# Performance work log

Hardware: AMD Instinct MI355X
Metric: run time of the kernel (lower is better)

## Reference

```python
import jax, jax.numpy as jnp
import numpy as np
from jax import lax

N_SAMPLES = 2 ** 15      # 32768
D_SIZE = 256             # number of dictionary atoms
KERNEL = 256             # atom length
N_STEPS = 16             # sparse_coding_iterations
CHANNELS = 128


def setup_inputs() -> dict:
    key = jax.random.key(0)
    ks = jax.random.split(key, 9)
    B = 8
    x = jax.random.normal(ks[0], (B, N_SAMPLES), dtype=jnp.float32)
    # dictionary, initialized uniform(-1, 1) as in nn.Parameter(...).uniform_(-1, 1)
    d = jax.random.uniform(ks[1], (D_SIZE, KERNEL), dtype=jnp.float32, minval=-1.0, maxval=1.0)
    # 1x1 Conv1d weights stored as (out, in); biases (out,)
    w_pos_amp = jax.random.normal(ks[2], (CHANNELS, 2), dtype=jnp.float32) * 0.1
    b_pos_amp = jnp.zeros((CHANNELS,), dtype=jnp.float32)
    w_atoms = jax.random.normal(ks[3], (CHANNELS, D_SIZE), dtype=jnp.float32) * 0.05
    b_atoms = jnp.zeros((CHANNELS,), dtype=jnp.float32)
    w_reduce = jax.random.normal(ks[4], (CHANNELS, 2 * CHANNELS), dtype=jnp.float32) * 0.05
    b_reduce = jnp.zeros((CHANNELS,), dtype=jnp.float32)
    return {
        'x': x, 'd': d,
        'w_pos_amp': w_pos_amp, 'b_pos_amp': b_pos_amp,
        'w_atoms': w_atoms, 'b_atoms': b_atoms,
        'w_reduce': w_reduce, 'b_reduce': b_reduce,
    }


def _correlate(residual, d):
    # residual: (B, 1, N), d: (D, K) -> feature map (B, D, N-K+1) (valid cross-correlation,
    # identical to torch F.conv1d with no padding)
    return lax.conv_general_dilated(
        residual, d[:, None, :], window_strides=(1,), padding='VALID',
        dimension_numbers=('NCH', 'OIH', 'NCH'))


def _matching_pursuit(x3, d):
    """16-step greedy matching pursuit. Returns key points (B, 2+D, N_STEPS) and residual."""
    B = x3.shape[0]
    T = N_SAMPLES - KERNEL + 1  # valid correlation length

    def step(residual, _):
        fm = _correlate(residual, d)                       # (B, D, T)
        flat = fm.reshape(B, -1)
        idx = jnp.argmax(jnp.abs(flat), axis=1)            # best (atom, pos) per example
        amp = jnp.take_along_axis(flat, idx[:, None], axis=1)[:, 0]
        atom_idx = idx // T
        pos = idx % T

        def subtract(r, p, ai, a):
            seg = lax.dynamic_slice(r, (p,), (KERNEL,))
            return lax.dynamic_update_slice(r, seg - a * d[ai], (p,))

        new_res = jax.vmap(subtract)(residual[:, 0, :], pos, atom_idx, amp)[:, None, :]
        enc = jnp.concatenate([
            (pos.astype(jnp.float32) / T)[:, None],        # normalized position
            amp[:, None],                                  # amplitude
            jax.nn.one_hot(atom_idx, D_SIZE, dtype=jnp.float32),  # atom one-hot
        ], axis=1)                                         # (B, 2+D)
        return new_res, enc

    residual, encs = lax.scan(step, x3, None, length=N_STEPS)  # encs: (S, B, 2+D)
    kp = jnp.transpose(encs, (1, 2, 0))                        # (B, 2+D, S)
    return kp, residual


def _conv1x1(w, b, x):
    # w: (O, C), x: (B, C, T) -> (B, O, T)
    return jnp.einsum('oc,bct->bot', w, x) + b[None, :, None]


def reference(x, d, w_pos_amp, b_pos_amp, w_atoms, b_atoms, w_reduce, b_reduce):
    B = x.shape[0]
    x3 = x.reshape(B, 1, N_SAMPLES)
    kp, _ = _matching_pursuit(x3, d)          # (B, 258, 16)
    pos_amp = kp[:, :2, :]
    atoms = kp[:, 2:, :]
    pa = _conv1x1(w_pos_amp, b_pos_amp, pos_amp)
    at = _conv1x1(w_atoms, b_atoms, atoms)
    h = jnp.concatenate([pa, at], axis=1)     # (B, 2*channels, 16)
    return _conv1x1(w_reduce, b_reduce, h)    # (B, channels, 16)
```

## Files before the change

### kernel.cpp

```cpp
#include <hip/hip_runtime.h>
#include <hip/hip_bf16.h>
#include <float.h>

#define NS 32768
#define KER 256
#define TOUT 32513
#define NATOM 256
#define NSTEP 16
#define BATCH 8
#define NBLK 255
#define XSTR 33024
#define SW4(i) ((i) + (((i) >> 5) << 2))

typedef __attribute__((ext_vector_type(8))) _Float16 half8;
typedef __attribute__((ext_vector_type(4))) float f32x4;
typedef __attribute__((ext_vector_type(4))) unsigned int uint4v;

__device__ __forceinline__ void cmax(float& ba, float& bs, float& bi,
                                     float oa, float os, float oi) {
    if (oa > ba || (oa == ba && oi < bi)) { ba = oa; bs = os; bi = oi; }
}

__device__ __forceinline__ void fma8(float acc[8], float4 dA, float4 dB,
                                     float4 w0, float4 w1, float4 w2, float4 w3) {
    float w[16] = {w0.x,w0.y,w0.z,w0.w, w1.x,w1.y,w1.z,w1.w,
                   w2.x,w2.y,w2.z,w2.w, w3.x,w3.y,w3.z,w3.w};
    float dv[8] = {dA.x,dA.y,dA.z,dA.w, dB.x,dB.y,dB.z,dB.w};
#pragma unroll
    for (int i = 0; i < 8; ++i)
#pragma unroll
        for (int j = 0; j < 8; ++j)
            acc[j] = fmaf(dv[i], w[i + j], acc[j]);
}

__global__ __launch_bounds__(256) void k_prep(const float* __restrict__ x,
                                              const float* __restrict__ d,
                                              unsigned int* __restrict__ xp,
                                              unsigned short* __restrict__ dh,
                                              unsigned short* __restrict__ dl) {
    const int gid = blockIdx.x * 256 + threadIdx.x;
    const int NX = BATCH * XSTR;
    if (gid < NX) {
        const int b = gid / XSTR, i = gid - b * XSTR;
        const float v = (i < NS) ? x[b * NS + i] : 0.f;
        const _Float16 h = (_Float16)v;
        const _Float16 lo = (_Float16)(v - (float)h);
        xp[gid] = ((unsigned int)__builtin_bit_cast(unsigned short, lo) << 16)
                | (unsigned int)__builtin_bit_cast(unsigned short, h);
    } else {
        const int j = gid - NX;
        if (j < NATOM * KER) {
            const float v = d[j];
            const _Float16 h = (_Float16)v;
            const _Float16 lo = (_Float16)(v - (float)h);
            dh[j] = __builtin_bit_cast(unsigned short, h);
            dl[j] = __builtin_bit_cast(unsigned short, lo);
        }
    }
}

__global__ __launch_bounds__(256) void k_init(const unsigned int* __restrict__ xp,
                                              const unsigned short* __restrict__ dh,
                                              const unsigned short* __restrict__ dl,
                                              float4* __restrict__ bm) {
    const int c = blockIdx.x, mg = blockIdx.y, b = blockIdx.z;
    const int tid = threadIdx.x;
    const int w = tid >> 6, l = tid & 63;
    const int l15 = l & 15, g = l >> 4;
    __shared__ unsigned int xw[512];
    __shared__ float4 wmax[4][16];
    const int t0 = c << 8;
    xw[tid] = xp[b * XSTR + t0 + tid];
    xw[tid + 256] = xp[b * XSTR + t0 + 256 + tid];
    __syncthreads();

    f32x4 acc0 = {0.f,0.f,0.f,0.f}, acc1 = {0.f,0.f,0.f,0.f};
    f32x4 acc2 = {0.f,0.f,0.f,0.f}, acc3 = {0.f,0.f,0.f,0.f};
    const int arow = (mg << 4) + l15;
    const unsigned short* dhp = dh + arow * 256 + (g << 3);
    const unsigned short* dlp = dl + arow * 256 + (g << 3);

#pragma unroll 2
    for (int kk = 0; kk < 8; ++kk) {
        const half8 ah = *(const half8*)(dhp + (kk << 5));
        const half8 al = *(const half8*)(dlp + (kk << 5));
        const int sbase = (w << 6) + (kk << 5) + l15 + (g << 3);
#pragma unroll
        for (int nt = 0; nt < 4; ++nt) {
            const int s = sbase + (nt << 4);
            const unsigned int w0 = xw[s],     w1 = xw[s + 1];
            const unsigned int w2 = xw[s + 2], w3 = xw[s + 3];
            const unsigned int w4 = xw[s + 4], w5 = xw[s + 5];
            const unsigned int w6 = xw[s + 6], w7 = xw[s + 7];
            uint4v hv = { (w0 & 0xffffu) | (w1 << 16),
                          (w2 & 0xffffu) | (w3 << 16),
                          (w4 & 0xffffu) | (w5 << 16),
                          (w6 & 0xffffu) | (w7 << 16) };
            uint4v lv = { (w0 >> 16) | (w1 & 0xffff0000u),
                          (w2 >> 16) | (w3 & 0xffff0000u),
                          (w4 >> 16) | (w5 & 0xffff0000u),
                          (w6 >> 16) | (w7 & 0xffff0000u) };
            const half8 bh = __builtin_bit_cast(half8, hv);
            const half8 bl = __builtin_bit_cast(half8, lv);
            f32x4 a = (nt == 0) ? acc0 : (nt == 1) ? acc1 : (nt == 2) ? acc2 : acc3;
            a = __builtin_amdgcn_mfma_f32_16x16x32_f16(ah, bl, a, 0, 0, 0);
            a = __builtin_amdgcn_mfma_f32_16x16x32_f16(al, bh, a, 0, 0, 0);
            a = __builtin_amdgcn_mfma_f32_16x16x32_f16(ah, bh, a, 0, 0, 0);
            if (nt == 0) acc0 = a; else if (nt == 1) acc1 = a;
            else if (nt == 2) acc2 = a; else acc3 = a;
        }
    }

#pragma unroll
    for (int r = 0; r < 4; ++r) {
        float ba = -1.f, bsg = 0.f, bi = 3.0e7f;
        const int atomg = (mg << 4) + (g << 2) + r;
#pragma unroll
        for (int nt = 0; nt < 4; ++nt) {
            const int t = t0 + (w << 6) + (nt << 4) + l15;
            const float v = (nt == 0) ? acc0[r] : (nt == 1) ? acc1[r]
                          : (nt == 2) ? acc2[r] : acc3[r];
            const float av = fabsf(v);
            if (t < TOUT && av > ba) { ba = av; bsg = v; bi = (float)(atomg * TOUT + t); }
        }
#pragma unroll
        for (int m = 1; m <= 8; m <<= 1) {
            float oa = __shfl_xor(ba, m, 16);
            float os = __shfl_xor(bsg, m, 16);
            float oi = __shfl_xor(bi, m, 16);
            cmax(ba, bsg, bi, oa, os, oi);
        }
        if (l15 == 0) wmax[w][(g << 2) + r] = make_float4(ba, bsg, bi, 0.f);
    }
    __syncthreads();
    if (tid < 32) {
        const int a = tid & 15, p = tid >> 4;
        float4 e1 = wmax[2 * p][a];
        const float4 e2 = wmax[2 * p + 1][a];
        float ba = e1.x, bsg = e1.y, bi = e1.z;
        cmax(ba, bsg, bi, e2.x, e2.y, e2.z);
        const int blk = (c << 1) + p;
        if (blk < NBLK)
            bm[(size_t)((b << 8) + (mg << 4) + a) * NBLK + blk] =
                make_float4(ba, bsg, bi, 0.f);
    }
}

__global__ __launch_bounds__(256) void k_lvl2(const float4* __restrict__ bm,
                                              float4* __restrict__ l2) {
    const int b = blockIdx.y;
    const int oglob = blockIdx.x * 8 + (threadIdx.x >> 5);
    const int lane = threadIdx.x & 31;
    const float4* row = bm + (size_t)(b * NATOM + oglob) * NBLK;
    float ba = -1.f, bsg = 0.f, bi = 3.0e7f;
    for (int i = lane; i < NBLK; i += 32) {
        float4 e = row[i];
        cmax(ba, bsg, bi, e.x, e.y, e.z);
    }
#pragma unroll
    for (int m = 16; m >= 1; m >>= 1) {
        float oa = __shfl_xor(ba, m, 32);
        float os = __shfl_xor(bsg, m, 32);
        float oi = __shfl_xor(bi, m, 32);
        cmax(ba, bsg, bi, oa, os, oi);
    }
    if (lane == 0) l2[(b << 8) + oglob] = make_float4(ba, bsg, bi, 0.f);
}

__global__ __launch_bounds__(512) void k_step(const float* __restrict__ x,
                                              const float* __restrict__ d,
                                              float4* __restrict__ bm,
                                              float4* __restrict__ l2,
                                              int* __restrict__ pos_a,
                                              int* __restrict__ atom_a,
                                              float* __restrict__ amp_a,
                                              int step) {
    const int og = blockIdx.x, b = blockIdx.y;
    const int tid = threadIdx.x;
    const int wave = tid >> 6, lane = tid & 63;
    __shared__ float dt[2048];
    __shared__ float rsu[1024];
    __shared__ float4 sred[8];
    __shared__ float4 upd[8][5];
    __shared__ int s_pos[NSTEP], s_atom[NSTEP];
    __shared__ float s_amp[NSTEP];

    ((float4*)dt)[tid] = ((const float4*)(d + og * 2048))[tid];
    if (tid < step) {
        s_pos[tid]  = pos_a[tid * BATCH + b];
        s_atom[tid] = atom_a[tid * BATCH + b];
        s_amp[tid]  = amp_a[tid * BATCH + b];
    }
    const float4* l2r = l2 + (step & 1) * (BATCH * NATOM);
    float4*       l2w = l2 + ((step + 1) & 1) * (BATCH * NATOM);

    {
        float ba = -1.f, bsg = 0.f, bi = 3.0e7f;
        if (tid < 256) {
            float4 e = l2r[(b << 8) + tid];
            ba = e.x; bsg = e.y; bi = e.z;
        }
#pragma unroll
        for (int m = 32; m >= 1; m >>= 1) {
            float oa = __shfl_xor(ba, m);
            float os = __shfl_xor(bsg, m);
            float oi = __shfl_xor(bi, m);
            cmax(ba, bsg, bi, oa, os, oi);
        }
        if (lane == 0) sred[wave] = make_float4(ba, bsg, bi, 0.f);
    }
    __syncthreads();
    if (tid == 0) {
        float4 r = sred[0];
#pragma unroll
        for (int i = 1; i < 8; ++i) {
            float4 q = sred[i];
            if (q.x > r.x || (q.x == r.x && q.z < r.z)) r = q;
        }
        const int idx = (int)r.z;
        const int atom = idx / TOUT;
        const int pos = idx - atom * TOUT;
        s_pos[step] = pos; s_atom[step] = atom; s_amp[step] = r.y;
        if (og == 0) {
            pos_a[step * BATCH + b] = pos;
            atom_a[step * BATCH + b] = atom;
            amp_a[step * BATCH + b] = r.y;
        }
    }
    __syncthreads();

    const int p = s_pos[step];
    int tlo = p - 255; if (tlo < 0) tlo = 0;
    int thi = p + 255; if (thi > TOUT - 1) thi = TOUT - 1;
    const int bs0 = tlo >> 7, be0 = thi >> 7;
    const int rbase = bs0 << 7;
    const int nblks = be0 - bs0 + 1;
    const int rlen = (nblks << 7) + 255;
    for (int i = tid; i < rlen; i += 512) {
        const int g = rbase + i;
        float v = (g < NS) ? x[(size_t)b * NS + g] : 0.f;
        for (int s2 = 0; s2 <= step; ++s2) {
            const int off = g - s_pos[s2];
            if (off >= 0 && off < KER)
                v = __fsub_rn(v, __fmul_rn(s_amp[s2], d[s_atom[s2] * KER + off]));
        }
        rsu[SW4(i)] = v;
    }
    __syncthreads();

    const int lg = lane >> 4, l16 = lane & 15;
    const float* dp = dt + (wave << 8) + (lg << 6);
    const int atomg = (og << 3) + wave;
    for (int bb = 0; bb < nblks; ++bb) {
        const int blk = bs0 + bb;
        const int t0r = (bb << 7) + (l16 << 3) + (lg << 6);
        float acc[8];
#pragma unroll
        for (int j = 0; j < 8; ++j) acc[j] = 0.f;
        float4 A0 = *(const float4*)(rsu + SW4(t0r));
        float4 A1 = *(const float4*)(rsu + SW4(t0r + 4));
        float4 B0 = *(const float4*)(rsu + SW4(t0r + 8));
        float4 B1 = *(const float4*)(rsu + SW4(t0r + 12));
#pragma unroll
        for (int kk = 0; kk < 64; kk += 16) {
            float4 d0 = *(const float4*)(dp + kk);
            float4 d1 = *(const float4*)(dp + kk + 4);
            float4 N0 = *(const float4*)(rsu + SW4(t0r + kk + 16));
            float4 N1 = *(const float4*)(rsu + SW4(t0r + kk + 20));
            fma8(acc, d0, d1, A0, A1, B0, B1);
            float4 d2 = *(const float4*)(dp + kk + 8);
            float4 d3 = *(const float4*)(dp + kk + 12);
            float4 M0 = *(const float4*)(rsu + SW4(t0r + kk + 24));
            float4 M1 = *(const float4*)(rsu + SW4(t0r + kk + 28));
            fma8(acc, d2, d3, B0, B1, N0, N1);
            A0 = N0; A1 = N1; B0 = M0; B1 = M1;
        }
#pragma unroll
        for (int j = 0; j < 8; ++j) {
            acc[j] += __shfl_xor(acc[j], 16);
            acc[j] += __shfl_xor(acc[j], 32);
        }
        float ba = -1.f, bsg = 0.f, bi = 3.0e7f;
        const int tb = rbase + (bb << 7) + (l16 << 3);
#pragma unroll
        for (int j = 0; j < 8; ++j) {
            const int t = tb + j;
            const float av = fabsf(acc[j]);
            if (t < TOUT && av > ba) { ba = av; bsg = acc[j]; bi = (float)(atomg * TOUT + t); }
        }
#pragma unroll
        for (int m = 32; m >= 1; m >>= 1) {
            float oa = __shfl_xor(ba, m);
            float os = __shfl_xor(bsg, m);
            float oi = __shfl_xor(bi, m);
            cmax(ba, bsg, bi, oa, os, oi);
        }
        if (lane == 0) {
            float4 e4 = make_float4(ba, bsg, bi, 0.f);
            bm[(size_t)(b * NATOM + atomg) * NBLK + blk] = e4;
            upd[wave][bb] = e4;
        }
    }
    __syncthreads();

    {
        float ba = -1.f, bsg = 0.f, bi = 3.0e7f;
        const float4* row = bm + (size_t)(b * NATOM + atomg) * NBLK;
        for (int i = lane; i < NBLK; i += 64) {
            float4 e2 = (i >= bs0 && i <= be0) ? upd[wave][i - bs0] : row[i];
            cmax(ba, bsg, bi, e2.x, e2.y, e2.z);
        }
#pragma unroll
        for (int m = 32; m >= 1; m >>= 1) {
            float oa = __shfl_xor(ba, m);
            float os = __shfl_xor(bsg, m);
            float oi = __shfl_xor(bi, m);
            cmax(ba, bsg, bi, oa, os, oi);
        }
        if (lane == 0) l2w[(b << 8) + atomg] = make_float4(ba, bsg, bi, 0.f);
    }
}

__global__ __launch_bounds__(128) void k_head(const int* __restrict__ pos_a,
                                              const int* __restrict__ atom_a,
                                              const float* __restrict__ amp_a,
                                              const float4* __restrict__ l2,
                                              const float* __restrict__ wpa,
                                              const float* __restrict__ bpa,
                                              const float* __restrict__ wat,
                                              const float* __restrict__ bat,
                                              const float* __restrict__ wr,
                                              const float* __restrict__ br,
                                              float* __restrict__ out) {
    const int s = blockIdx.x, b = blockIdx.y;
    const int o = threadIdx.x;
    __shared__ float4 hred[2];
    __shared__ int sh_pos, sh_atom;
    __shared__ float sh_amp;
    int pos, atom; float amp;
    if (s == NSTEP - 1) {
        const float4* l2r = l2 + ((NSTEP - 1) & 1) * (BATCH * NATOM);
        float ba = -1.f, bsg = 0.f, bi = 3.0e7f;
        float4 e0 = l2r[(b << 8) + o];
        float4 e1 = l2r[(b << 8) + 128 + o];
        cmax(ba, bsg, bi, e0.x, e0.y, e0.z);
        cmax(ba, bsg, bi, e1.x, e1.y, e1.z);
#pragma unroll
        for (int m = 32; m >= 1; m >>= 1) {
            float oa = __shfl_xor(ba, m);
            float os = __shfl_xor(bsg, m);
            float oi = __shfl_xor(bi, m);
            cmax(ba, bsg, bi, oa, os, oi);
        }
        if ((o & 63) == 0) hred[o >> 6] = make_float4(ba, bsg, bi, 0.f);
        __syncthreads();
        if (o == 0) {
            float4 r = hred[0], q = hred[1];
            if (q.x > r.x || (q.x == r.x && q.z < r.z)) r = q;
            const int idx = (int)r.z;
            sh_atom = idx / TOUT;
            sh_pos = idx - sh_atom * TOUT;
            sh_amp = r.y;
        }
        __syncthreads();
        pos = sh_pos; atom = sh_atom; amp = sh_amp;
    } else {
        pos  = pos_a[s * BATCH + b];
        atom = atom_a[s * BATCH + b];
        amp  = amp_a[s * BATCH + b];
    }
    const float posn = (float)pos / 32513.0f;
    float sum = br[o];
    for (int c = 0; c < 128; ++c) {
        float pa = wpa[c * 2] * posn + wpa[c * 2 + 1] * amp + bpa[c];
        float at = wat[c * 256 + atom] + bat[c];
        sum += wr[o * 256 + c] * pa + wr[o * 256 + 128 + c] * at;
    }
    out[(b * 128 + o) * NSTEP + s] = sum;
}

extern "C" void kernel_launch(void* const* d_in, const int* in_sizes, int n_in,
                              void* d_out, int out_size, void* d_ws, size_t ws_size,
                              hipStream_t stream) {
    const float* x   = (const float*)d_in[0];
    const float* d   = (const float*)d_in[1];
    const float* wpa = (const float*)d_in[2];
    const float* bpa = (const float*)d_in[3];
    const float* wat = (const float*)d_in[4];
    const float* bat = (const float*)d_in[5];
    const float* wr  = (const float*)d_in[6];
    const float* br  = (const float*)d_in[7];
    float* out = (float*)d_out;

    char* ws = (char*)d_ws;
    float4* bm = (float4*)ws;
    float4* l2 = (float4*)(ws + 8355840);
    int*   pos_a  = (int*)(ws + 8355840 + 65536);
    int*   atom_a = pos_a + NSTEP * BATCH;
    float* amp_a  = (float*)(atom_a + NSTEP * BATCH);
    unsigned int*   xp = (unsigned int*)(ws + 8355840 + 65536 + 512);
    unsigned short* dh = (unsigned short*)(ws + 8355840 + 65536 + 512 + 1056768);
    unsigned short* dl = dh + NATOM * KER;

    const int prep_n = BATCH * XSTR + NATOM * KER;
    k_prep<<<(prep_n + 255) / 256, 256, 0, stream>>>(x, d, xp, dh, dl);
    k_init<<<dim3(128, 16, 8), 256, 0, stream>>>(xp, dh, dl, bm);
    k_lvl2<<<dim3(32, 8), 256, 0, stream>>>(bm, l2);
    for (int st = 0; st < NSTEP - 1; ++st)
        k_step<<<dim3(32, 8), 512, 0, stream>>>(x, d, bm, l2, pos_a, atom_a, amp_a, st);
    k_head<<<dim3(16, 8), 128, 0, stream>>>(pos_a, atom_a, amp_a, l2,
                                            wpa, bpa, wat, bat, wr, br, out);
}
```

Baseline: 433.6 us.

## Use 32x32 MFMA in init, shrink block-max records, ping-pong materialized residual

The initial correlation kernel now uses 32x32x16 fp16 MFMAs over 32-atom groups, reading x from split hi/lo uint2 planes and d from a pre-swizzled layout. Per-block max records shrink from float4 to float2, with the absolute value recomputed on read, which halves bm traffic. The step kernel no longer replays every prior subtraction from x. It keeps a materialized residual in two ping-pong buffers, and each launch copies and updates it with only the current atom. This adds a full residual copy per step and a device-to-device memcpy at the start, in exchange for removing the O(step) replay loop.

```diff
diff --git a/kernel.cpp b/kernel.cpp
--- a/kernel.cpp
+++ b/kernel.cpp
@@ -13,7 +13,7 @@
 #define SW4(i) ((i) + (((i) >> 5) << 2))
 
 typedef __attribute__((ext_vector_type(8))) _Float16 half8;
-typedef __attribute__((ext_vector_type(4))) float f32x4;
+typedef __attribute__((ext_vector_type(16))) float f32x16;
 typedef __attribute__((ext_vector_type(4))) unsigned int uint4v;
 
 __device__ __forceinline__ void cmax(float& ba, float& bs, float& bi,
@@ -33,143 +33,166 @@
             acc[j] = fmaf(dv[i], w[i + j], acc[j]);
 }
 
+__device__ __forceinline__ unsigned short f16hi(float v) {
+    return __builtin_bit_cast(unsigned short, (_Float16)v);
+}
+__device__ __forceinline__ unsigned short f16lo(float v) {
+    const _Float16 h = (_Float16)v;
+    return __builtin_bit_cast(unsigned short, (_Float16)(v - (float)h));
+}
+
 __global__ __launch_bounds__(256) void k_prep(const float* __restrict__ x,
                                               const float* __restrict__ d,
-                                              unsigned int* __restrict__ xp,
-                                              unsigned short* __restrict__ dh,
-                                              unsigned short* __restrict__ dl) {
+                                              uint2* __restrict__ xh4,
+                                              uint2* __restrict__ xl4,
+                                              uint4* __restrict__ dhF,
+                                              uint4* __restrict__ dlF) {
     const int gid = blockIdx.x * 256 + threadIdx.x;
-    const int NX = BATCH * XSTR;
-    if (gid < NX) {
+    const int NXE = BATCH * XSTR;
+    if (gid < NXE) {
         const int b = gid / XSTR, i = gid - b * XSTR;
-        const float v = (i < NS) ? x[b * NS + i] : 0.f;
-        const _Float16 h = (_Float16)v;
-        const _Float16 lo = (_Float16)(v - (float)h);
-        xp[gid] = ((unsigned int)__builtin_bit_cast(unsigned short, lo) << 16)
-                | (unsigned int)__builtin_bit_cast(unsigned short, h);
+        float v[4];
+#pragma unroll
+        for (int u = 0; u < 4; ++u)
+            v[u] = (i + u < NS) ? x[b * NS + i + u] : 0.f;
+        uint2 hw, lw;
+        hw.x = (unsigned int)f16hi(v[0]) | ((unsigned int)f16hi(v[1]) << 16);
+        hw.y = (unsigned int)f16hi(v[2]) | ((unsigned int)f16hi(v[3]) << 16);
+        lw.x = (unsigned int)f16lo(v[0]) | ((unsigned int)f16lo(v[1]) << 16);
+        lw.y = (unsigned int)f16lo(v[2]) | ((unsigned int)f16lo(v[3]) << 16);
+        xh4[gid] = hw; xl4[gid] = lw;
     } else {
-        const int j = gid - NX;
-        if (j < NATOM * KER) {
-            const float v = d[j];
-            const _Float16 h = (_Float16)v;
-            const _Float16 lo = (_Float16)(v - (float)h);
-            dh[j] = __builtin_bit_cast(unsigned short, h);
-            dl[j] = __builtin_bit_cast(unsigned short, lo);
-        }
-    }
-}
-
-__global__ __launch_bounds__(256) void k_init(const unsigned int* __restrict__ xp,
-                                              const unsigned short* __restrict__ dh,
-                                              const unsigned short* __restrict__ dl,
-                                              float4* __restrict__ bm) {
+        const int j = gid - NXE;
+        if (j < NATOM * 32) {
+            const int kg = j >> 8, atom = j & 255;
+            const float* dp = d + atom * 256 + (kg << 3);
+            uint4 hw, lw;
+            hw.x = (unsigned int)f16hi(dp[0]) | ((unsigned int)f16hi(dp[1]) << 16);
+            hw.y = (unsigned int)f16hi(dp[2]) | ((unsigned int)f16hi(dp[3]) << 16);
+            hw.z = (unsigned int)f16hi(dp[4]) | ((unsigned int)f16hi(dp[5]) << 16);
+            hw.w = (unsigned int)f16hi(dp[6]) | ((unsigned int)f16hi(dp[7]) << 16);
+            lw.x = (unsigned int)f16lo(dp[0]) | ((unsigned int)f16lo(dp[1]) << 16);
+            lw.y = (unsigned int)f16lo(dp[2]) | ((unsigned int)f16lo(dp[3]) << 16);
+            lw.z = (unsigned int)f16lo(dp[4]) | ((unsigned int)f16lo(dp[5]) << 16);
+            lw.w = (unsigned int)f16lo(dp[6]) | ((unsigned int)f16lo(dp[7]) << 16);
+            dhF[(kg << 8) + atom] = hw;
+            dlF[(kg << 8) + atom] = lw;
+        }
+    }
+}
+
+__global__ __launch_bounds__(256) void k_init(const uint2* __restrict__ xh4,
+                                              const uint2* __restrict__ xl4,
+                                              const uint4* __restrict__ dhF,
+                                              const uint4* __restrict__ dlF,
+                                              float2* __restrict__ bm) {
     const int c = blockIdx.x, mg = blockIdx.y, b = blockIdx.z;
     const int tid = threadIdx.x;
     const int w = tid >> 6, l = tid & 63;
-    const int l15 = l & 15, g = l >> 4;
-    __shared__ unsigned int xw[512];
-    __shared__ float4 wmax[4][16];
+    const int n = l & 31, h = l >> 5;
+    __shared__ uint2 xh[512], xl[512];
+    __shared__ float4 wmax[4][32];
     const int t0 = c << 8;
-    xw[tid] = xp[b * XSTR + t0 + tid];
-    xw[tid + 256] = xp[b * XSTR + t0 + 256 + tid];
-    __syncthreads();
-
-    f32x4 acc0 = {0.f,0.f,0.f,0.f}, acc1 = {0.f,0.f,0.f,0.f};
-    f32x4 acc2 = {0.f,0.f,0.f,0.f}, acc3 = {0.f,0.f,0.f,0.f};
-    const int arow = (mg << 4) + l15;
-    const unsigned short* dhp = dh + arow * 256 + (g << 3);
-    const unsigned short* dlp = dl + arow * 256 + (g << 3);
-
+    for (int i = tid; i < 512; i += 256) {
+        xh[i] = xh4[b * XSTR + t0 + i];
+        xl[i] = xl4[b * XSTR + t0 + i];
+    }
+    __syncthreads();
+
+    const int arow = (mg << 5) + n;
+    f32x16 acc0 = {0.f}, acc1 = {0.f};
+#pragma unroll
+    for (int j = 0; j < 16; ++j) { acc0[j] = 0.f; acc1[j] = 0.f; }
+    const int sb = (w << 6) + n + (h << 3);
 #pragma unroll 2
-    for (int kk = 0; kk < 8; ++kk) {
-        const half8 ah = *(const half8*)(dhp + (kk << 5));
-        const half8 al = *(const half8*)(dlp + (kk << 5));
-        const int sbase = (w << 6) + (kk << 5) + l15 + (g << 3);
-#pragma unroll
-        for (int nt = 0; nt < 4; ++nt) {
-            const int s = sbase + (nt << 4);
-            const unsigned int w0 = xw[s],     w1 = xw[s + 1];
-            const unsigned int w2 = xw[s + 2], w3 = xw[s + 3];
-            const unsigned int w4 = xw[s + 4], w5 = xw[s + 5];
-            const unsigned int w6 = xw[s + 6], w7 = xw[s + 7];
-            uint4v hv = { (w0 & 0xffffu) | (w1 << 16),
-                          (w2 & 0xffffu) | (w3 << 16),
-                          (w4 & 0xffffu) | (w5 << 16),
-                          (w6 & 0xffffu) | (w7 << 16) };
-            uint4v lv = { (w0 >> 16) | (w1 & 0xffff0000u),
-                          (w2 >> 16) | (w3 & 0xffff0000u),
-                          (w4 >> 16) | (w5 & 0xffff0000u),
-                          (w6 >> 16) | (w7 & 0xffff0000u) };
+    for (int kk = 0; kk < 16; ++kk) {
+        const int kg = (kk << 1) + h;
+        const half8 ah = __builtin_bit_cast(half8, dhF[(kg << 8) + arow]);
+        const half8 al = __builtin_bit_cast(half8, dlF[(kg << 8) + arow]);
+        const int s0 = sb + (kk << 4);
+        {
+            const uint2 h0 = xh[s0], h1 = xh[s0 + 4];
+            const uint2 l0 = xl[s0], l1 = xl[s0 + 4];
+            const uint4v hv = {h0.x, h0.y, h1.x, h1.y};
+            const uint4v lv = {l0.x, l0.y, l1.x, l1.y};
             const half8 bh = __builtin_bit_cast(half8, hv);
             const half8 bl = __builtin_bit_cast(half8, lv);
-            f32x4 a = (nt == 0) ? acc0 : (nt == 1) ? acc1 : (nt == 2) ? acc2 : acc3;
-            a = __builtin_amdgcn_mfma_f32_16x16x32_f16(ah, bl, a, 0, 0, 0);
-            a = __builtin_amdgcn_mfma_f32_16x16x32_f16(al, bh, a, 0, 0, 0);
-            a = __builtin_amdgcn_mfma_f32_16x16x32_f16(ah, bh, a, 0, 0, 0);
-            if (nt == 0) acc0 = a; else if (nt == 1) acc1 = a;
-            else if (nt == 2) acc2 = a; else acc3 = a;
-        }
-    }
-
-#pragma unroll
-    for (int r = 0; r < 4; ++r) {
+            acc0 = __builtin_amdgcn_mfma_f32_32x32x16_f16(ah, bl, acc0, 0, 0, 0);
+            acc0 = __builtin_amdgcn_mfma_f32_32x32x16_f16(al, bh, acc0, 0, 0, 0);
+            acc0 = __builtin_amdgcn_mfma_f32_32x32x16_f16(ah, bh, acc0, 0, 0, 0);
+        }
+        {
+            const uint2 h0 = xh[s0 + 32], h1 = xh[s0 + 36];
+            const uint2 l0 = xl[s0 + 32], l1 = xl[s0 + 36];
+            const uint4v hv = {h0.x, h0.y, h1.x, h1.y};
+            const uint4v lv = {l0.x, l0.y, l1.x, l1.y};
+            const half8 bh = __builtin_bit_cast(half8, hv);
+            const half8 bl = __builtin_bit_cast(half8, lv);
+            acc1 = __builtin_amdgcn_mfma_f32_32x32x16_f16(ah, bl, acc1, 0, 0, 0);
+            acc1 = __builtin_amdgcn_mfma_f32_32x32x16_f16(al, bh, acc1, 0, 0, 0);
+            acc1 = __builtin_amdgcn_mfma_f32_32x32x16_f16(ah, bh, acc1, 0, 0, 0);
+        }
+    }
+
+    const int tb0 = t0 + (w << 6) + n;
+#pragma unroll
+    for (int r = 0; r < 16; ++r) {
+        const int atom_l = (r & 3) + ((r >> 2) << 3) + (h << 2);
+        const float fa = (float)(((mg << 5) + atom_l) * TOUT);
         float ba = -1.f, bsg = 0.f, bi = 3.0e7f;
-        const int atomg = (mg << 4) + (g << 2) + r;
-#pragma unroll
-        for (int nt = 0; nt < 4; ++nt) {
-            const int t = t0 + (w << 6) + (nt << 4) + l15;
-            const float v = (nt == 0) ? acc0[r] : (nt == 1) ? acc1[r]
-                          : (nt == 2) ? acc2[r] : acc3[r];
-            const float av = fabsf(v);
-            if (t < TOUT && av > ba) { ba = av; bsg = v; bi = (float)(atomg * TOUT + t); }
-        }
-#pragma unroll
-        for (int m = 1; m <= 8; m <<= 1) {
-            float oa = __shfl_xor(ba, m, 16);
-            float os = __shfl_xor(bsg, m, 16);
-            float oi = __shfl_xor(bi, m, 16);
+        const float v0 = acc0[r], v1 = acc1[r];
+        if (tb0 < TOUT) { ba = fabsf(v0); bsg = v0; bi = fa + (float)tb0; }
+        if (tb0 + 32 < TOUT) {
+            const float a1 = fabsf(v1);
+            if (a1 > ba) { ba = a1; bsg = v1; bi = fa + (float)(tb0 + 32); }
+        }
+#pragma unroll
+        for (int m = 1; m <= 16; m <<= 1) {
+            const float oa = __shfl_xor(ba, m, 32);
+            const float os = __shfl_xor(bsg, m, 32);
+            const float oi = __shfl_xor(bi, m, 32);
             cmax(ba, bsg, bi, oa, os, oi);
         }
-        if (l15 == 0) wmax[w][(g << 2) + r] = make_float4(ba, bsg, bi, 0.f);
-    }
-    __syncthreads();
-    if (tid < 32) {
-        const int a = tid & 15, p = tid >> 4;
-        float4 e1 = wmax[2 * p][a];
-        const float4 e2 = wmax[2 * p + 1][a];
+        if (n == 0) wmax[w][atom_l] = make_float4(ba, bsg, bi, 0.f);
+    }
+    __syncthreads();
+    if (tid < 64) {
+        const int a = tid & 31, p = tid >> 5;
+        const float4 e1 = wmax[(p << 1)][a];
+        const float4 e2 = wmax[(p << 1) + 1][a];
         float ba = e1.x, bsg = e1.y, bi = e1.z;
         cmax(ba, bsg, bi, e2.x, e2.y, e2.z);
         const int blk = (c << 1) + p;
         if (blk < NBLK)
-            bm[(size_t)((b << 8) + (mg << 4) + a) * NBLK + blk] =
-                make_float4(ba, bsg, bi, 0.f);
-    }
-}
-
-__global__ __launch_bounds__(256) void k_lvl2(const float4* __restrict__ bm,
+            bm[(size_t)((b << 8) + (mg << 5) + a) * NBLK + blk] = make_float2(bsg, bi);
+    }
+}
+
+__global__ __launch_bounds__(256) void k_lvl2(const float2* __restrict__ bm,
                                               float4* __restrict__ l2) {
     const int b = blockIdx.y;
     const int oglob = blockIdx.x * 8 + (threadIdx.x >> 5);
     const int lane = threadIdx.x & 31;
-    const float4* row = bm + (size_t)(b * NATOM + oglob) * NBLK;
+    const float2* row = bm + (size_t)(b * NATOM + oglob) * NBLK;
     float ba = -1.f, bsg = 0.f, bi = 3.0e7f;
     for (int i = lane; i < NBLK; i += 32) {
-        float4 e = row[i];
-        cmax(ba, bsg, bi, e.x, e.y, e.z);
+        const float2 e = row[i];
+        cmax(ba, bsg, bi, fabsf(e.x), e.x, e.y);
     }
 #pragma unroll
     for (int m = 16; m >= 1; m >>= 1) {
-        float oa = __shfl_xor(ba, m, 32);
-        float os = __shfl_xor(bsg, m, 32);
-        float oi = __shfl_xor(bi, m, 32);
+        const float oa = __shfl_xor(ba, m, 32);
+        const float os = __shfl_xor(bsg, m, 32);
+        const float oi = __shfl_xor(bi, m, 32);
         cmax(ba, bsg, bi, oa, os, oi);
     }
     if (lane == 0) l2[(b << 8) + oglob] = make_float4(ba, bsg, bi, 0.f);
 }
 
-__global__ __launch_bounds__(512) void k_step(const float* __restrict__ x,
-                                              const float* __restrict__ d,
-                                              float4* __restrict__ bm,
+__global__ __launch_bounds__(512) void k_step(const float* __restrict__ d,
+                                              const float* __restrict__ resid_src,
+                                              float* __restrict__ resid_dst,
+                                              float2* __restrict__ bm,
                                               float4* __restrict__ l2,
                                               int* __restrict__ pos_a,
                                               int* __restrict__ atom_a,
@@ -182,29 +205,24 @@
     __shared__ float rsu[1024];
     __shared__ float4 sred[8];
     __shared__ float4 upd[8][5];
-    __shared__ int s_pos[NSTEP], s_atom[NSTEP];
-    __shared__ float s_amp[NSTEP];
+    __shared__ int sh_pos, sh_atom;
+    __shared__ float sh_amp;
 
     ((float4*)dt)[tid] = ((const float4*)(d + og * 2048))[tid];
-    if (tid < step) {
-        s_pos[tid]  = pos_a[tid * BATCH + b];
-        s_atom[tid] = atom_a[tid * BATCH + b];
-        s_amp[tid]  = amp_a[tid * BATCH + b];
-    }
     const float4* l2r = l2 + (step & 1) * (BATCH * NATOM);
     float4*       l2w = l2 + ((step + 1) & 1) * (BATCH * NATOM);
 
     {
         float ba = -1.f, bsg = 0.f, bi = 3.0e7f;
         if (tid < 256) {
-            float4 e = l2r[(b << 8) + tid];
+            const float4 e = l2r[(b << 8) + tid];
             ba = e.x; bsg = e.y; bi = e.z;
         }
 #pragma unroll
         for (int m = 32; m >= 1; m >>= 1) {
-            float oa = __shfl_xor(ba, m);
-            float os = __shfl_xor(bsg, m);
-            float oi = __shfl_xor(bi, m);
+            const float oa = __shfl_xor(ba, m);
+            const float os = __shfl_xor(bsg, m);
+            const float oi = __shfl_xor(bi, m);
             cmax(ba, bsg, bi, oa, os, oi);
         }
         if (lane == 0) sred[wave] = make_float4(ba, bsg, bi, 0.f);
@@ -214,13 +232,13 @@
         float4 r = sred[0];
 #pragma unroll
         for (int i = 1; i < 8; ++i) {
-            float4 q = sred[i];
+            const float4 q = sred[i];
             if (q.x > r.x || (q.x == r.x && q.z < r.z)) r = q;
         }
         const int idx = (int)r.z;
         const int atom = idx / TOUT;
         const int pos = idx - atom * TOUT;
-        s_pos[step] = pos; s_atom[step] = atom; s_amp[step] = r.y;
+        sh_pos = pos; sh_atom = atom; sh_amp = r.y;
         if (og == 0) {
             pos_a[step * BATCH + b] = pos;
             atom_a[step * BATCH + b] = atom;
@@ -228,8 +246,18 @@
         }
     }
     __syncthreads();
-
-    const int p = s_pos[step];
+    const int p = sh_pos, atom_s = sh_atom;
+    const float amp = sh_amp;
+
+    for (int i = tid; i < 1024; i += 512) {
+        const int g = (og << 10) + i;
+        float v = resid_src[(size_t)b * NS + g];
+        const int off = g - p;
+        if (off >= 0 && off < KER)
+            v = __fsub_rn(v, __fmul_rn(amp, d[atom_s * KER + off]));
+        resid_dst[(size_t)b * NS + g] = v;
+    }
+
     int tlo = p - 255; if (tlo < 0) tlo = 0;
     int thi = p + 255; if (thi > TOUT - 1) thi = TOUT - 1;
     const int bs0 = tlo >> 7, be0 = thi >> 7;
@@ -238,12 +266,10 @@
     const int rlen = (nblks << 7) + 255;
     for (int i = tid; i < rlen; i += 512) {
         const int g = rbase + i;
-        float v = (g < NS) ? x[(size_t)b * NS + g] : 0.f;
-        for (int s2 = 0; s2 <= step; ++s2) {
-            const int off = g - s_pos[s2];
-            if (off >= 0 && off < KER)
-                v = __fsub_rn(v, __fmul_rn(s_amp[s2], d[s_atom[s2] * KER + off]));
-        }
+        float v = (g < NS) ? resid_src[(size_t)b * NS + g] : 0.f;
+        const int off = g - p;
+        if (g < NS && off >= 0 && off < KER)
+            v = __fsub_rn(v, __fmul_rn(amp, d[atom_s * KER + off]));
         rsu[SW4(i)] = v;
     }
     __syncthreads();
@@ -263,15 +289,15 @@
         float4 B1 = *(const float4*)(rsu + SW4(t0r + 12));
 #pragma unroll
         for (int kk = 0; kk < 64; kk += 16) {
-            float4 d0 = *(const float4*)(dp + kk);
-            float4 d1 = *(const float4*)(dp + kk + 4);
-            float4 N0 = *(const float4*)(rsu + SW4(t0r + kk + 16));
-            float4 N1 = *(const float4*)(rsu + SW4(t0r + kk + 20));
+            const float4 d0 = *(const float4*)(dp + kk);
+            const float4 d1 = *(const float4*)(dp + kk + 4);
+            const float4 N0 = *(const float4*)(rsu + SW4(t0r + kk + 16));
+            const float4 N1 = *(const float4*)(rsu + SW4(t0r + kk + 20));
             fma8(acc, d0, d1, A0, A1, B0, B1);
-            float4 d2 = *(const float4*)(dp + kk + 8);
-            float4 d3 = *(const float4*)(dp + kk + 12);
-            float4 M0 = *(const float4*)(rsu + SW4(t0r + kk + 24));
-            float4 M1 = *(const float4*)(rsu + SW4(t0r + kk + 28));
+            const float4 d2 = *(const float4*)(dp + kk + 8);
+            const float4 d3 = *(const float4*)(dp + kk + 12);
+            const float4 M0 = *(const float4*)(rsu + SW4(t0r + kk + 24));
+            const float4 M1 = *(const float4*)(rsu + SW4(t0r + kk + 28));
             fma8(acc, d2, d3, B0, B1, N0, N1);
             A0 = N0; A1 = N1; B0 = M0; B1 = M1;
         }
@@ -281,40 +307,44 @@
             acc[j] += __shfl_xor(acc[j], 32);
         }
         float ba = -1.f, bsg = 0.f, bi = 3.0e7f;
-        const int tb = rbase + (bb << 7) + (l16 << 3);
+        const int tbp = rbase + (bb << 7) + (l16 << 3);
 #pragma unroll
         for (int j = 0; j < 8; ++j) {
-            const int t = tb + j;
+            const int t = tbp + j;
             const float av = fabsf(acc[j]);
             if (t < TOUT && av > ba) { ba = av; bsg = acc[j]; bi = (float)(atomg * TOUT + t); }
         }
 #pragma unroll
         for (int m = 32; m >= 1; m >>= 1) {
-            float oa = __shfl_xor(ba, m);
-            float os = __shfl_xor(bsg, m);
-            float oi = __shfl_xor(bi, m);
+            const float oa = __shfl_xor(ba, m);
+            const float os = __shfl_xor(bsg, m);
+            const float oi = __shfl_xor(bi, m);
             cmax(ba, bsg, bi, oa, os, oi);
         }
         if (lane == 0) {
-            float4 e4 = make_float4(ba, bsg, bi, 0.f);
-            bm[(size_t)(b * NATOM + atomg) * NBLK + blk] = e4;
-            upd[wave][bb] = e4;
+            bm[(size_t)(b * NATOM + atomg) * NBLK + blk] = make_float2(bsg, bi);
+            upd[wave][bb] = make_float4(ba, bsg, bi, 0.f);
         }
     }
     __syncthreads();
 
     {
         float ba = -1.f, bsg = 0.f, bi = 3.0e7f;
-        const float4* row = bm + (size_t)(b * NATOM + atomg) * NBLK;
+        const float2* row = bm + (size_t)(b * NATOM + atomg) * NBLK;
         for (int i = lane; i < NBLK; i += 64) {
-            float4 e2 = (i >= bs0 && i <= be0) ? upd[wave][i - bs0] : row[i];
-            cmax(ba, bsg, bi, e2.x, e2.y, e2.z);
+            if (i >= bs0 && i <= be0) {
+                const float4 e2 = upd[wave][i - bs0];
+                cmax(ba, bsg, bi, e2.x, e2.y, e2.z);
+            } else {
+                const float2 e2 = row[i];
+                cmax(ba, bsg, bi, fabsf(e2.x), e2.x, e2.y);
+            }
         }
 #pragma unroll
         for (int m = 32; m >= 1; m >>= 1) {
-            float oa = __shfl_xor(ba, m);
-            float os = __shfl_xor(bsg, m);
-            float oi = __shfl_xor(bi, m);
+            const float oa = __shfl_xor(ba, m);
+            const float os = __shfl_xor(bsg, m);
+            const float oi = __shfl_xor(bi, m);
             cmax(ba, bsg, bi, oa, os, oi);
         }
         if (lane == 0) l2w[(b << 8) + atomg] = make_float4(ba, bsg, bi, 0.f);
@@ -341,21 +371,22 @@
     if (s == NSTEP - 1) {
         const float4* l2r = l2 + ((NSTEP - 1) & 1) * (BATCH * NATOM);
         float ba = -1.f, bsg = 0.f, bi = 3.0e7f;
-        float4 e0 = l2r[(b << 8) + o];
-        float4 e1 = l2r[(b << 8) + 128 + o];
+        const float4 e0 = l2r[(b << 8) + o];
+        const float4 e1 = l2r[(b << 8) + 128 + o];
         cmax(ba, bsg, bi, e0.x, e0.y, e0.z);
         cmax(ba, bsg, bi, e1.x, e1.y, e1.z);
 #pragma unroll
         for (int m = 32; m >= 1; m >>= 1) {
-            float oa = __shfl_xor(ba, m);
-            float os = __shfl_xor(bsg, m);
-            float oi = __shfl_xor(bi, m);
+            const float oa = __shfl_xor(ba, m);
+            const float os = __shfl_xor(bsg, m);
+            const float oi = __shfl_xor(bi, m);
             cmax(ba, bsg, bi, oa, os, oi);
         }
         if ((o & 63) == 0) hred[o >> 6] = make_float4(ba, bsg, bi, 0.f);
         __syncthreads();
         if (o == 0) {
-            float4 r = hred[0], q = hred[1];
+            float4 r = hred[0];
+            const float4 q = hred[1];
             if (q.x > r.x || (q.x == r.x && q.z < r.z)) r = q;
             const int idx = (int)r.z;
             sh_atom = idx / TOUT;
@@ -372,8 +403,8 @@
     const float posn = (float)pos / 32513.0f;
     float sum = br[o];
     for (int c = 0; c < 128; ++c) {
-        float pa = wpa[c * 2] * posn + wpa[c * 2 + 1] * amp + bpa[c];
-        float at = wat[c * 256 + atom] + bat[c];
+        const float pa = wpa[c * 2] * posn + wpa[c * 2 + 1] * amp + bpa[c];
+        const float at = wat[c * 256 + atom] + bat[c];
         sum += wr[o * 256 + c] * pa + wr[o * 256 + 128 + c] * at;
     }
     out[(b * 128 + o) * NSTEP + s] = sum;
@@ -393,21 +424,30 @@
     float* out = (float*)d_out;
 
     char* ws = (char*)d_ws;
-    float4* bm = (float4*)ws;
-    float4* l2 = (float4*)(ws + 8355840);
-    int*   pos_a  = (int*)(ws + 8355840 + 65536);
-    int*   atom_a = pos_a + NSTEP * BATCH;
-    float* amp_a  = (float*)(atom_a + NSTEP * BATCH);
-    unsigned int*   xp = (unsigned int*)(ws + 8355840 + 65536 + 512);
-    unsigned short* dh = (unsigned short*)(ws + 8355840 + 65536 + 512 + 1056768);
-    unsigned short* dl = dh + NATOM * KER;
-
-    const int prep_n = BATCH * XSTR + NATOM * KER;
-    k_prep<<<(prep_n + 255) / 256, 256, 0, stream>>>(x, d, xp, dh, dl);
-    k_init<<<dim3(128, 16, 8), 256, 0, stream>>>(xp, dh, dl, bm);
+    float2* bm     = (float2*)ws;
+    float4* l2     = (float4*)(ws + 4177920);
+    int*    pos_a  = (int*)(ws + 4243456);
+    int*    atom_a = (int*)(ws + 4243968);
+    float*  amp_a  = (float*)(ws + 4244480);
+    float*  resid0 = (float*)(ws + 4244992);
+    float*  resid1 = (float*)(ws + 5293568);
+    uint2*  xh4    = (uint2*)(ws + 6342144);
+    uint2*  xl4    = (uint2*)(ws + 8455680);
+    uint4*  dhF    = (uint4*)(ws + 10569216);
+    uint4*  dlF    = (uint4*)(ws + 10700288);
+
+    hipMemcpyAsync(resid0, x, (size_t)BATCH * NS * sizeof(float),
+                   hipMemcpyDeviceToDevice, stream);
+    const int prep_n = BATCH * XSTR + NATOM * 32;
+    k_prep<<<(prep_n + 255) / 256, 256, 0, stream>>>(x, d, xh4, xl4, dhF, dlF);
+    k_init<<<dim3(128, 8, 8), 256, 0, stream>>>(xh4, xl4, dhF, dlF, bm);
     k_lvl2<<<dim3(32, 8), 256, 0, stream>>>(bm, l2);
-    for (int st = 0; st < NSTEP - 1; ++st)
-        k_step<<<dim3(32, 8), 512, 0, stream>>>(x, d, bm, l2, pos_a, atom_a, amp_a, st);
+    for (int st = 0; st < NSTEP - 1; ++st) {
+        float* rs = (st & 1) ? resid1 : resid0;
+        float* rd = (st & 1) ? resid0 : resid1;
+        k_step<<<dim3(32, 8), 512, 0, stream>>>(d, rs, rd, bm, l2,
+                                                pos_a, atom_a, amp_a, st);
+    }
     k_head<<<dim3(16, 8), 128, 0, stream>>>(pos_a, atom_a, amp_a, l2,
                                             wpa, bpa, wat, bat, wr, br, out);
 }
```

Result: slower. 443.2 us (+2.2%).
